# Kernel tuning notes

Measured on AMD Instinct MI355X. Metric: run time of the kernel, lower is better.

The kernel has to match this reference:

```python
import jax, jax.numpy as jnp
import numpy as np

DIM = 256          # channels C
RC = DIM // 8      # reduction_dim = max(dim//8, 4) = 32
K_RATE = 0.75


def setup_inputs() -> dict:
    key = jax.random.key(0)
    ks = jax.random.split(key, 8)
    B, C, H, W = 2, DIM, 64, 64
    rc = RC
    return {
        "x": jax.random.normal(ks[0], (B, C, H, W), jnp.float32),
        "mix_param": jnp.zeros((1,), jnp.float32),                                  # nn.Parameter(zeros(1))
        "w_red": jax.random.normal(ks[1], (rc, C), jnp.float32) * (2.0 / C) ** 0.5,  # conv1x1 kaiming
        "b_red": jnp.zeros((rc,), jnp.float32),
        "w_qkv": jax.random.normal(ks[2], (3 * rc, rc), jnp.float32) * rc ** -0.5,
        "b_qkv": jnp.zeros((3 * rc,), jnp.float32),
        "w_s1": jax.random.normal(ks[3], (C // 2, C), jnp.float32) * C ** -0.5,
        "b_s1": jnp.zeros((C // 2,), jnp.float32),
        "w_s2": jax.random.normal(ks[4], (1, C // 2), jnp.float32) * (C // 2) ** -0.5,
        "b_s2": jnp.zeros((1,), jnp.float32),
    }


def _pool2(x):
    # MaxPool2d(2,2) and AvgPool2d(2,2) on NCHW
    dims, strides = (1, 1, 2, 2), (1, 1, 2, 2)
    mx = jax.lax.reduce_window(x, -jnp.inf, jax.lax.max, dims, strides, 'VALID')
    av = jax.lax.reduce_window(x, 0.0, jax.lax.add, dims, strides, 'VALID') * 0.25
    return mx, av


def _attention(xg, w_red, b_red, w_qkv, b_qkv):
    # xg: [B2, C, h, w]
    B2, C, h, w = xg.shape
    rc = w_red.shape[0]
    S = h * w
    # 1x1 conv channel reduction
    xr = jnp.einsum('bchw,rc->brhw', xg, w_red) + b_red[None, :, None, None]
    xf = xr.reshape(B2, rc, S).transpose(0, 2, 1)             # [B2, S, rc]
    qkv = xf @ w_qkv.T + b_qkv                                # [B2, S, 3*rc]
    q, k, v = qkv[..., :rc], qkv[..., rc:2 * rc], qkv[..., 2 * rc:]
    scores = jnp.einsum('bsr,btr->bst', q, k) / jnp.sqrt(jnp.float32(rc))
    scores = jnp.where(jnp.isnan(scores), -jnp.inf, scores)
    kv = max(1, int(S * K_RATE))                              # static top-k size
    top_vals, top_idx = jax.lax.top_k(scores, kv)             # [B2, S, kv]
    weights = jax.nn.softmax(top_vals, axis=-1)
    # per-(b,s) gather of v rows, then weighted sum over the kv selected keys
    gathered = jax.vmap(lambda vv, ii: vv[ii])(v, top_idx)    # [B2, S, kv, rc]
    out = jnp.einsum('bsk,bskr->bsr', weights, gathered)      # [B2, S, rc]
    out = out.transpose(0, 2, 1).reshape(B2, rc, h, w)
    # re-projection: conv2d with transposed channel_reduction weight, no bias
    return jnp.einsum('brhw,rc->bchw', out, w_red)


def _gating(xg, w_s1, b_s1, w_s2, b_s2):
    # eval-mode gate: hard threshold of sigmoid(score MLP(GAP(x)))
    pooled = xg.mean(axis=(2, 3))                             # [B2, C]
    h1 = jax.nn.relu(pooled @ w_s1.T + b_s1)
    gate_score = jax.nn.sigmoid(h1 @ w_s2.T + b_s2)           # [B2, 1]
    gate = (gate_score > 0.5).astype(xg.dtype)[:, :, None, None]
    return gate * xg


def reference(x, mix_param, w_red, b_red, w_qkv, b_qkv, w_s1, b_s1, w_s2, b_s2):
    mx, av = _pool2(x)
    mw = jax.nn.sigmoid(mix_param)                            # lerp weight, shape [1]
    x1 = mx + mw * (av - mx)                                  # torch.lerp(max, avg, w)
    x2 = av + mw * (mx - av)                                  # torch.lerp(avg, max, w)
    B, C, h, w = x1.shape
    combined = jnp.stack([x1, x2], axis=1).reshape(B * 2, C, h, w)
    attn_out = _attention(combined, w_red, b_red, w_qkv, b_qkv)   # [2B, C, h, w]
    gated = _gating(combined, w_s1, b_s1, w_s2, b_s2).reshape(B, 2, C, h, w)
    out = jnp.maximum(gated[:, 0], gated[:, 1])               # [B, C, h, w]
    return out, attn_out
```

## Files before the change

### kernel.cpp

```cpp
#include <hip/hip_runtime.h>

#define CC 256
#define RC 32
#define SS 1024
#define KV 768

__global__ void k_pool_mix(const float* __restrict__ x, const float* __restrict__ mixp,
                           float* __restrict__ comb, float* __restrict__ pooled) {
    int tid = threadIdx.x;
    int idx = blockIdx.x * 256 + tid;
    int ow = idx & 31, t = idx >> 5;
    int oh = t & 31;  t >>= 5;
    int c = t & 255;  int b = t >> 8;
    const float* px = x + (((size_t)(b*CC + c)*64 + oh*2)*64 + ow*2);
    float2 r0 = *(const float2*)px;
    float2 r1 = *(const float2*)(px + 64);
    float mx = fmaxf(fmaxf(r0.x, r0.y), fmaxf(r1.x, r1.y));
    float av = 0.25f*(r0.x + r0.y + r1.x + r1.y);
    float mw = 1.f/(1.f + expf(-mixp[0]));
    float x1 = mx + mw*(av - mx);
    float x2 = av + mw*(mx - av);
    int s = oh*32 + ow;
    comb[((size_t)(b*2+0)*CC + c)*SS + s] = x1;
    comb[((size_t)(b*2+1)*CC + c)*SS + s] = x2;
    __shared__ float red[256];
    red[tid] = x1; __syncthreads();
    for (int off = 128; off; off >>= 1) { if (tid < off) red[tid] += red[tid+off]; __syncthreads(); }
    if (tid == 0) atomicAdd(&pooled[(b*2)*CC + c], red[0]);
    __syncthreads();
    red[tid] = x2; __syncthreads();
    for (int off = 128; off; off >>= 1) { if (tid < off) red[tid] += red[tid+off]; __syncthreads(); }
    if (tid == 0) atomicAdd(&pooled[(b*2+1)*CC + c], red[0]);
}

__global__ void k_gate(const float* __restrict__ pooled, const float* __restrict__ w_s1,
                       const float* __restrict__ b_s1, const float* __restrict__ w_s2,
                       const float* __restrict__ b_s2, float* __restrict__ gate) {
    int b2 = blockIdx.x; int j = threadIdx.x;
    const float* pl = pooled + b2 * CC;
    float acc = 0.f;
    for (int c = 0; c < CC; c++) acc += pl[c] * w_s1[j*CC + c];
    float h1 = fmaxf(acc * (1.f/1024.f) + b_s1[j], 0.f);
    __shared__ float red[128];
    red[j] = h1 * w_s2[j]; __syncthreads();
    for (int off = 64; off; off >>= 1) { if (j < off) red[j] += red[j+off]; __syncthreads(); }
    if (j == 0) gate[b2] = (red[0] + b_s2[0] > 0.f) ? 1.f : 0.f;
}

__global__ void k_out0(const float* __restrict__ comb, const float* __restrict__ gate,
                       float* __restrict__ out) {
    int idx = blockIdx.x * 256 + threadIdx.x;
    int s = idx & 1023;
    int t = idx >> 10;
    int c = t & 255; int b = t >> 8;
    float g0 = gate[b*2+0], g1 = gate[b*2+1];
    float v0 = g0 * comb[((size_t)(b*2+0)*CC + c)*SS + s];
    float v1 = g1 * comb[((size_t)(b*2+1)*CC + c)*SS + s];
    out[idx] = fmaxf(v0, v1);
}

__global__ __launch_bounds__(256) void k_qkv(
        const float* __restrict__ comb, const float* __restrict__ w_red,
        const float* __restrict__ b_red, const float* __restrict__ w_qkv,
        const float* __restrict__ b_qkv,
        float* __restrict__ q, float* __restrict__ k, float* __restrict__ v) {
    __shared__ float wredT[CC*33];
    __shared__ float wqP[96*33];
    int tid = threadIdx.x;
    int b2 = blockIdx.x >> 6; int tile = blockIdx.x & 63; int s0 = tile*16;
    for (int i = tid; i < CC*RC; i += 256) { int r = i >> 8, c = i & 255; wredT[c*33 + r] = w_red[i]; }
    for (int i = tid; i < 96*RC; i += 256) { int j = i >> 5, r = i & 31; wqP[j*33 + r] = w_qkv[i]; }
    __syncthreads();
    int s_loc = tid >> 4, p = tid & 15;
    int s = s0 + s_loc;
    float xf[RC];
    #pragma unroll
    for (int r = 0; r < RC; r++) xf[r] = 0.f;
    const float* pc = comb + (size_t)(b2*CC)*SS + s;
    #pragma unroll
    for (int ci = 0; ci < 16; ci++) {
        int c = p + 16*ci;
        float val = pc[(size_t)c * SS];
        #pragma unroll
        for (int r = 0; r < RC; r++) xf[r] += val * wredT[c*33 + r];
    }
    #pragma unroll
    for (int m1 = 1; m1 <= 8; m1 <<= 1) {
        #pragma unroll
        for (int r = 0; r < RC; r++) xf[r] += __shfl_xor(xf[r], m1);
    }
    #pragma unroll
    for (int r = 0; r < RC; r++) xf[r] += b_red[r];
    size_t base = (size_t)(b2*SS + s)*RC;
    #pragma unroll
    for (int jj = 0; jj < 6; jj++) {
        int j = p*6 + jj;
        float acc = b_qkv[j];
        #pragma unroll
        for (int r = 0; r < RC; r++) acc += xf[r]*wqP[j*33 + r];
        if      (j < 32) q[base + j]      = acc;
        else if (j < 64) k[base + j - 32] = acc;
        else             v[base + j - 64] = acc;
    }
}

__global__ __launch_bounds__(256, 1) void k_attn(
        const float* __restrict__ qg, const float* __restrict__ kg,
        const float* __restrict__ vg, float* __restrict__ mid) {
    __shared__ float Ks[128*36];
    int tid = threadIdx.x;
    int b2 = blockIdx.x >> 6; int tile = blockIdx.x & 63;
    int r = tid >> 4, c = tid & 15;
    int grow = b2*SS + tile*16 + r;

    float qreg[RC];
    { const float4* qp = (const float4*)(qg + (size_t)grow*RC);
      #pragma unroll
      for (int i = 0; i < 8; i++) { float4 t4 = qp[i]; qreg[4*i]=t4.x; qreg[4*i+1]=t4.y; qreg[4*i+2]=t4.z; qreg[4*i+3]=t4.w; } }

    const float4* ksrc = (const float4*)(kg + (size_t)(b2*SS)*RC);
    const float4* vsrc = (const float4*)(vg + (size_t)(b2*SS)*RC);
    float4 stg[4];
    #pragma unroll
    for (int kk = 0; kk < 4; kk++) stg[kk] = ksrc[tid + 256*kk];

    unsigned int u[64];
    float lmax = -INFINITY;
    const float scale = 0.17677669529663687f;

    #pragma unroll
    for (int ch = 0; ch < 8; ch++) {
        __syncthreads();
        #pragma unroll
        for (int kk = 0; kk < 4; kk++) {
            int idx4 = tid + 256*kk;
            *(float4*)&Ks[(idx4 >> 3)*36 + (idx4 & 7)*4] = stg[kk];
        }
        __syncthreads();
        if (ch < 7) {
            #pragma unroll
            for (int kk = 0; kk < 4; kk++) stg[kk] = ksrc[(ch+1)*1024 + tid + 256*kk];
        } else {
            #pragma unroll
            for (int kk = 0; kk < 4; kk++) stg[kk] = vsrc[tid + 256*kk];
        }
        #pragma unroll
        for (int qq = 0; qq < 8; qq++) {
            int cl = c + 16*qq;
            const float4* kr = (const float4*)&Ks[cl*36];
            float a0=0.f, a1=0.f, a2=0.f, a3=0.f;
            #pragma unroll
            for (int k4 = 0; k4 < 8; k4++) {
                float4 kv4 = kr[k4];
                a0 += qreg[4*k4]*kv4.x;   a1 += qreg[4*k4+1]*kv4.y;
                a2 += qreg[4*k4+2]*kv4.z; a3 += qreg[4*k4+3]*kv4.w;
            }
            float d = ((a0+a1)+(a2+a3))*scale;
            if (d != d) d = -INFINITY;
            lmax = fmaxf(lmax, d);
            unsigned int bb = __float_as_uint(d);
            u[ch*8+qq] = bb ^ ((bb & 0x80000000u) ? 0xFFFFFFFFu : 0x80000000u);
        }
    }

    #pragma unroll
    for (int m1 = 1; m1 <= 8; m1 <<= 1) lmax = fmaxf(lmax, __shfl_xor(lmax, m1));
    float m = lmax;

    unsigned int p = 0u, utau = 0u; bool found = false;
    for (int bit = 31; bit >= 0; --bit) {
        if (found) break;
        unsigned int cand = p | (1u << bit);
        int cnt = 0;
        #pragma unroll
        for (int i = 0; i < 64; i++) cnt += (u[i] >= cand) ? 1 : 0;
        #pragma unroll
        for (int m1 = 1; m1 <= 8; m1 <<= 1) cnt += __shfl_xor(cnt, m1);
        if (cnt >= KV) {
            if (cnt == KV) {
                unsigned int um = 0xFFFFFFFFu;
                #pragma unroll
                for (int i = 0; i < 64; i++) if (u[i] >= cand && u[i] < um) um = u[i];
                #pragma unroll
                for (int m1 = 1; m1 <= 8; m1 <<= 1) {
                    unsigned int o = (unsigned int)__shfl_xor((int)um, m1);
                    um = (o < um) ? o : um;
                }
                utau = um; found = true;
            } else p = cand;
        }
    }
    if (!found) utau = p;

    int cg = 0, eqc = 0;
    #pragma unroll
    for (int i = 0; i < 64; i++) { cg += (u[i] > utau) ? 1 : 0; eqc += (u[i] == utau) ? 1 : 0; }
    #pragma unroll
    for (int m1 = 1; m1 <= 8; m1 <<= 1) { cg += __shfl_xor(cg, m1); eqc += __shfl_xor(eqc, m1); }
    int extra = KV - cg;

    float w[64]; float den = 0.f;
    if (extra == eqc) {
        #pragma unroll
        for (int i = 0; i < 64; i++) {
            bool sel = (u[i] >= utau);
            unsigned int bb = u[i] ^ ((u[i] & 0x80000000u) ? 0x80000000u : 0xFFFFFFFFu);
            float wv = sel ? expf(__uint_as_float(bb) - m) : 0.f;
            w[i] = wv; den += wv;
        }
    } else {
        int prior = 0;
        #pragma unroll
        for (int i = 0; i < 64; i++) {
            bool eq = (u[i] == utau);
            unsigned long long bm = __ballot(eq);
            unsigned int bm16 = (unsigned int)((bm >> (tid & 48)) & 0xFFFFull);
            int rank = prior + __popc(bm16 & ((1u << c) - 1u));
            prior += __popc(bm16);
            bool sel = (u[i] > utau) || (eq && rank < extra);
            unsigned int bb = u[i] ^ ((u[i] & 0x80000000u) ? 0x80000000u : 0xFFFFFFFFu);
            float wv = sel ? expf(__uint_as_float(bb) - m) : 0.f;
            w[i] = wv; den += wv;
        }
    }
    #pragma unroll
    for (int m1 = 1; m1 <= 8; m1 <<= 1) den += __shfl_xor(den, m1);

    float acc[RC];
    #pragma unroll
    for (int i = 0; i < RC; i++) acc[i] = 0.f;
    #pragma unroll
    for (int ch = 0; ch < 8; ch++) {
        __syncthreads();
        #pragma unroll
        for (int kk = 0; kk < 4; kk++) {
            int idx4 = tid + 256*kk;
            *(float4*)&Ks[(idx4 >> 3)*36 + (idx4 & 7)*4] = stg[kk];
        }
        __syncthreads();
        if (ch < 7) {
            #pragma unroll
            for (int kk = 0; kk < 4; kk++) stg[kk] = vsrc[(ch+1)*1024 + tid + 256*kk];
        }
        #pragma unroll
        for (int qq = 0; qq < 8; qq++) {
            int cl = c + 16*qq;
            float wj = w[ch*8 + qq];
            const float4* vr = (const float4*)&Ks[cl*36];
            #pragma unroll
            for (int k4 = 0; k4 < 8; k4++) {
                float4 vv = vr[k4];
                acc[4*k4]   += wj*vv.x; acc[4*k4+1] += wj*vv.y;
                acc[4*k4+2] += wj*vv.z; acc[4*k4+3] += wj*vv.w;
            }
        }
    }
    #pragma unroll
    for (int m1 = 1; m1 <= 8; m1 <<= 1) {
        #pragma unroll
        for (int i = 0; i < RC; i++) acc[i] += __shfl_xor(acc[i], m1);
    }
    if (c == 0) {
        float rden = 1.f/den;
        float4* dst = (float4*)(mid + (size_t)grow*RC);
        #pragma unroll
        for (int k4 = 0; k4 < 8; k4++)
            dst[k4] = make_float4(acc[4*k4]*rden, acc[4*k4+1]*rden, acc[4*k4+2]*rden, acc[4*k4+3]*rden);
    }
}

__global__ __launch_bounds__(256) void k_proj(
        const float* __restrict__ mid, const float* __restrict__ w_red,
        float* __restrict__ attn_out) {
    __shared__ float wr[32*32];
    int tid = threadIdx.x;
    int b2 = blockIdx.x >> 5; int st = (blockIdx.x >> 3) & 3; int cch = blockIdx.x & 7;
    for (int i = tid; i < 1024; i += 256) {
        int rr = i >> 5, cc = i & 31;
        wr[i] = w_red[rr*CC + cch*32 + cc];
    }
    __syncthreads();
    int s = st*256 + tid;
    float xr[RC];
    const float4* mp = (const float4*)(mid + (size_t)(b2*SS + s)*RC);
    #pragma unroll
    for (int i = 0; i < 8; i++) { float4 t4 = mp[i]; xr[4*i]=t4.x; xr[4*i+1]=t4.y; xr[4*i+2]=t4.z; xr[4*i+3]=t4.w; }
    #pragma unroll
    for (int cc = 0; cc < 32; cc++) {
        float a = 0.f;
        #pragma unroll
        for (int rr = 0; rr < RC; rr++) a += xr[rr]*wr[rr*32 + cc];
        attn_out[((size_t)(b2*CC) + cch*32 + cc)*SS + s] = a;
    }
}

extern "C" void kernel_launch(void* const* d_in, const int* in_sizes, int n_in,
                              void* d_out, int out_size, void* d_ws, size_t ws_size,
                              hipStream_t stream) {
    const float* x     = (const float*)d_in[0];
    const float* mixp  = (const float*)d_in[1];
    const float* w_red = (const float*)d_in[2];
    const float* b_red = (const float*)d_in[3];
    const float* w_qkv = (const float*)d_in[4];
    const float* b_qkv = (const float*)d_in[5];
    const float* w_s1  = (const float*)d_in[6];
    const float* b_s1  = (const float*)d_in[7];
    const float* w_s2  = (const float*)d_in[8];
    const float* b_s2  = (const float*)d_in[9];
    float* out = (float*)d_out;

    float* ws     = (float*)d_ws;
    float* comb   = ws;
    float* q      = comb + 1048576;
    float* k      = q + 131072;
    float* v      = k + 131072;
    float* mid    = v + 131072;
    float* pooled = mid + 131072;
    float* gate   = pooled + 1024;

    hipMemsetAsync(pooled, 0, 1024*sizeof(float), stream);
    k_pool_mix<<<2048, 256, 0, stream>>>(x, mixp, comb, pooled);
    k_gate    <<<4,    128, 0, stream>>>(pooled, w_s1, b_s1, w_s2, b_s2, gate);
    k_out0    <<<2048, 256, 0, stream>>>(comb, gate, out);
    k_qkv     <<<256,  256, 0, stream>>>(comb, w_red, b_red, w_qkv, b_qkv, q, k, v);
    k_attn    <<<256,  256, 0, stream>>>(q, k, v, mid);
    k_proj    <<<128,  256, 0, stream>>>(mid, w_red, out + 524288);
}
```

Before: 182.3 us.

## Fuse gating into qkv/proj kernels and use one wavefront per attention row

The pooling kernel now has one block per (batch, channel) and writes the pooled sums directly, which removes the memset and the atomics. The gate MLP runs in four extra blocks of the qkv kernel, and the gated-max output is folded into the projection kernel, cutting the launch count from six to four. The attention kernel now gives each query row one 64-lane wavefront that reads K and V straight from global memory, with no shared-memory staging and no barriers, and runs more blocks per CU. It finishes with a butterfly transpose-reduction of the accumulators instead of the full per-element shuffle reductions. The trade-off is more redundant global/L2 reads of K and V, one per row instead of one per 16-row tile.

```diff
diff --git a/kernel.cpp b/kernel.cpp
--- a/kernel.cpp
+++ b/kernel.cpp
@@ -5,84 +5,94 @@
 #define SS 1024
 #define KV 768
 
-__global__ void k_pool_mix(const float* __restrict__ x, const float* __restrict__ mixp,
-                           float* __restrict__ comb, float* __restrict__ pooled) {
+__global__ __launch_bounds__(256) void k_pool(const float* __restrict__ x,
+                                              const float* __restrict__ mixp,
+                                              float* __restrict__ comb,
+                                              float* __restrict__ pooled) {
+    int bid = blockIdx.x;
+    int b = bid >> 8, c = bid & 255;
     int tid = threadIdx.x;
-    int idx = blockIdx.x * 256 + tid;
-    int ow = idx & 31, t = idx >> 5;
-    int oh = t & 31;  t >>= 5;
-    int c = t & 255;  int b = t >> 8;
-    const float* px = x + (((size_t)(b*CC + c)*64 + oh*2)*64 + ow*2);
-    float2 r0 = *(const float2*)px;
-    float2 r1 = *(const float2*)(px + 64);
-    float mx = fmaxf(fmaxf(r0.x, r0.y), fmaxf(r1.x, r1.y));
-    float av = 0.25f*(r0.x + r0.y + r1.x + r1.y);
-    float mw = 1.f/(1.f + expf(-mixp[0]));
-    float x1 = mx + mw*(av - mx);
-    float x2 = av + mw*(mx - av);
-    int s = oh*32 + ow;
-    comb[((size_t)(b*2+0)*CC + c)*SS + s] = x1;
-    comb[((size_t)(b*2+1)*CC + c)*SS + s] = x2;
-    __shared__ float red[256];
-    red[tid] = x1; __syncthreads();
-    for (int off = 128; off; off >>= 1) { if (tid < off) red[tid] += red[tid+off]; __syncthreads(); }
-    if (tid == 0) atomicAdd(&pooled[(b*2)*CC + c], red[0]);
+    int wid = tid >> 6, lane = tid & 63;
+    const float* base = x + (size_t)(b * CC + c) * 4096;
+    float mw = 1.f / (1.f + expf(-mixp[0]));
+    float* c1 = comb + ((size_t)(b * 2 + 0) * CC + c) * SS;
+    float* c2 = comb + ((size_t)(b * 2 + 1) * CC + c) * SS;
+    float ls1 = 0.f, ls2 = 0.f;
+    #pragma unroll
+    for (int it = 0; it < 4; it++) {
+        int s = tid + 256 * it;
+        int oh = s >> 5, ow = s & 31;
+        const float* px = base + (oh * 2) * 64 + ow * 2;
+        float2 r0 = *(const float2*)px;
+        float2 r1 = *(const float2*)(px + 64);
+        float mx = fmaxf(fmaxf(r0.x, r0.y), fmaxf(r1.x, r1.y));
+        float av = 0.25f * (r0.x + r0.y + r1.x + r1.y);
+        float x1 = mx + mw * (av - mx);
+        float x2 = av + mw * (mx - av);
+        c1[s] = x1; c2[s] = x2;
+        ls1 += x1; ls2 += x2;
+    }
+    #pragma unroll
+    for (int off = 32; off; off >>= 1) {
+        ls1 += __shfl_xor(ls1, off);
+        ls2 += __shfl_xor(ls2, off);
+    }
+    __shared__ float sred[2][4];
+    if (lane == 0) { sred[0][wid] = ls1; sred[1][wid] = ls2; }
     __syncthreads();
-    red[tid] = x2; __syncthreads();
-    for (int off = 128; off; off >>= 1) { if (tid < off) red[tid] += red[tid+off]; __syncthreads(); }
-    if (tid == 0) atomicAdd(&pooled[(b*2+1)*CC + c], red[0]);
-}
-
-__global__ void k_gate(const float* __restrict__ pooled, const float* __restrict__ w_s1,
-                       const float* __restrict__ b_s1, const float* __restrict__ w_s2,
-                       const float* __restrict__ b_s2, float* __restrict__ gate) {
-    int b2 = blockIdx.x; int j = threadIdx.x;
-    const float* pl = pooled + b2 * CC;
-    float acc = 0.f;
-    for (int c = 0; c < CC; c++) acc += pl[c] * w_s1[j*CC + c];
-    float h1 = fmaxf(acc * (1.f/1024.f) + b_s1[j], 0.f);
-    __shared__ float red[128];
-    red[j] = h1 * w_s2[j]; __syncthreads();
-    for (int off = 64; off; off >>= 1) { if (j < off) red[j] += red[j+off]; __syncthreads(); }
-    if (j == 0) gate[b2] = (red[0] + b_s2[0] > 0.f) ? 1.f : 0.f;
-}
-
-__global__ void k_out0(const float* __restrict__ comb, const float* __restrict__ gate,
-                       float* __restrict__ out) {
-    int idx = blockIdx.x * 256 + threadIdx.x;
-    int s = idx & 1023;
-    int t = idx >> 10;
-    int c = t & 255; int b = t >> 8;
-    float g0 = gate[b*2+0], g1 = gate[b*2+1];
-    float v0 = g0 * comb[((size_t)(b*2+0)*CC + c)*SS + s];
-    float v1 = g1 * comb[((size_t)(b*2+1)*CC + c)*SS + s];
-    out[idx] = fmaxf(v0, v1);
+    if (tid == 0) {
+        pooled[(b * 2 + 0) * CC + c] = sred[0][0] + sred[0][1] + sred[0][2] + sred[0][3];
+        pooled[(b * 2 + 1) * CC + c] = sred[1][0] + sred[1][1] + sred[1][2] + sred[1][3];
+    }
 }
 
 __global__ __launch_bounds__(256) void k_qkv(
         const float* __restrict__ comb, const float* __restrict__ w_red,
         const float* __restrict__ b_red, const float* __restrict__ w_qkv,
         const float* __restrict__ b_qkv,
+        const float* __restrict__ pooled, const float* __restrict__ w_s1,
+        const float* __restrict__ b_s1, const float* __restrict__ w_s2,
+        const float* __restrict__ b_s2, float* __restrict__ gate,
         float* __restrict__ q, float* __restrict__ k, float* __restrict__ v) {
-    __shared__ float wredT[CC*33];
-    __shared__ float wqP[96*33];
+    __shared__ float wredT[CC * 33];
+    __shared__ float wqP[96 * 33];
+    __shared__ float gred[128];
     int tid = threadIdx.x;
-    int b2 = blockIdx.x >> 6; int tile = blockIdx.x & 63; int s0 = tile*16;
-    for (int i = tid; i < CC*RC; i += 256) { int r = i >> 8, c = i & 255; wredT[c*33 + r] = w_red[i]; }
-    for (int i = tid; i < 96*RC; i += 256) { int j = i >> 5, r = i & 31; wqP[j*33 + r] = w_qkv[i]; }
+    if (blockIdx.x >= 256) {
+        int b2 = blockIdx.x - 256;
+        if (tid < 128) {
+            const float* pl = pooled + b2 * CC;
+            float acc = 0.f;
+            for (int c = 0; c < CC; c++) acc += pl[c] * w_s1[tid * CC + c];
+            float h1 = fmaxf(acc * (1.f / 1024.f) + b_s1[tid], 0.f);
+            gred[tid] = h1 * w_s2[tid];
+        }
+        __syncthreads();
+        if (tid < 64) gred[tid] += gred[tid + 64];
+        __syncthreads();
+        if (tid == 0) {
+            float sum = 0.f;
+            for (int i = 0; i < 64; i++) sum += gred[i];
+            gate[b2] = (sum + b_s2[0] > 0.f) ? 1.f : 0.f;
+        }
+        return;
+    }
+    int b2 = blockIdx.x >> 6; int tile = blockIdx.x & 63; int s0 = tile * 16;
+    for (int i = tid; i < CC * RC; i += 256) { int r = i >> 8, c = i & 255; wredT[c * 33 + r] = w_red[i]; }
+    for (int i = tid; i < 96 * RC; i += 256) { int j = i >> 5, r = i & 31; wqP[j * 33 + r] = w_qkv[i]; }
     __syncthreads();
     int s_loc = tid >> 4, p = tid & 15;
     int s = s0 + s_loc;
     float xf[RC];
     #pragma unroll
     for (int r = 0; r < RC; r++) xf[r] = 0.f;
-    const float* pc = comb + (size_t)(b2*CC)*SS + s;
+    const float* pc = comb + (size_t)(b2 * CC) * SS + s;
     #pragma unroll
     for (int ci = 0; ci < 16; ci++) {
-        int c = p + 16*ci;
+        int c = p + 16 * ci;
         float val = pc[(size_t)c * SS];
         #pragma unroll
-        for (int r = 0; r < RC; r++) xf[r] += val * wredT[c*33 + r];
+        for (int r = 0; r < RC; r++) xf[r] += val * wredT[c * 33 + r];
     }
     #pragma unroll
     for (int m1 = 1; m1 <= 8; m1 <<= 1) {
@@ -91,80 +101,56 @@
     }
     #pragma unroll
     for (int r = 0; r < RC; r++) xf[r] += b_red[r];
-    size_t base = (size_t)(b2*SS + s)*RC;
+    size_t base = (size_t)(b2 * SS + s) * RC;
     #pragma unroll
     for (int jj = 0; jj < 6; jj++) {
-        int j = p*6 + jj;
+        int j = p * 6 + jj;
         float acc = b_qkv[j];
         #pragma unroll
-        for (int r = 0; r < RC; r++) acc += xf[r]*wqP[j*33 + r];
+        for (int r = 0; r < RC; r++) acc += xf[r] * wqP[j * 33 + r];
         if      (j < 32) q[base + j]      = acc;
         else if (j < 64) k[base + j - 32] = acc;
         else             v[base + j - 64] = acc;
     }
 }
 
-__global__ __launch_bounds__(256, 1) void k_attn(
+__global__ __launch_bounds__(256, 4) void k_attn(
         const float* __restrict__ qg, const float* __restrict__ kg,
         const float* __restrict__ vg, float* __restrict__ mid) {
-    __shared__ float Ks[128*36];
     int tid = threadIdx.x;
-    int b2 = blockIdx.x >> 6; int tile = blockIdx.x & 63;
-    int r = tid >> 4, c = tid & 15;
-    int grow = b2*SS + tile*16 + r;
+    int wid = tid >> 6, lane = tid & 63;
+    int row = blockIdx.x * 4 + wid;
+    int b2 = row >> 10;
+    const float* kbase = kg + ((size_t)b2 << 10) * RC;
+    const float* vbase = vg + ((size_t)b2 << 10) * RC;
 
     float qreg[RC];
-    { const float4* qp = (const float4*)(qg + (size_t)grow*RC);
+    { const float4* qp = (const float4*)(qg + (size_t)row * RC);
       #pragma unroll
-      for (int i = 0; i < 8; i++) { float4 t4 = qp[i]; qreg[4*i]=t4.x; qreg[4*i+1]=t4.y; qreg[4*i+2]=t4.z; qreg[4*i+3]=t4.w; } }
-
-    const float4* ksrc = (const float4*)(kg + (size_t)(b2*SS)*RC);
-    const float4* vsrc = (const float4*)(vg + (size_t)(b2*SS)*RC);
-    float4 stg[4];
-    #pragma unroll
-    for (int kk = 0; kk < 4; kk++) stg[kk] = ksrc[tid + 256*kk];
-
-    unsigned int u[64];
+      for (int i = 0; i < 8; i++) { float4 t = qp[i]; qreg[4*i]=t.x; qreg[4*i+1]=t.y; qreg[4*i+2]=t.z; qreg[4*i+3]=t.w; } }
+
+    const float scale = 0.17677669529663687f;
+    unsigned int u[16];
     float lmax = -INFINITY;
-    const float scale = 0.17677669529663687f;
-
-    #pragma unroll
-    for (int ch = 0; ch < 8; ch++) {
-        __syncthreads();
-        #pragma unroll
-        for (int kk = 0; kk < 4; kk++) {
-            int idx4 = tid + 256*kk;
-            *(float4*)&Ks[(idx4 >> 3)*36 + (idx4 & 7)*4] = stg[kk];
-        }
-        __syncthreads();
-        if (ch < 7) {
-            #pragma unroll
-            for (int kk = 0; kk < 4; kk++) stg[kk] = ksrc[(ch+1)*1024 + tid + 256*kk];
-        } else {
-            #pragma unroll
-            for (int kk = 0; kk < 4; kk++) stg[kk] = vsrc[tid + 256*kk];
-        }
-        #pragma unroll
-        for (int qq = 0; qq < 8; qq++) {
-            int cl = c + 16*qq;
-            const float4* kr = (const float4*)&Ks[cl*36];
-            float a0=0.f, a1=0.f, a2=0.f, a3=0.f;
-            #pragma unroll
-            for (int k4 = 0; k4 < 8; k4++) {
-                float4 kv4 = kr[k4];
-                a0 += qreg[4*k4]*kv4.x;   a1 += qreg[4*k4+1]*kv4.y;
-                a2 += qreg[4*k4+2]*kv4.z; a3 += qreg[4*k4+3]*kv4.w;
-            }
-            float d = ((a0+a1)+(a2+a3))*scale;
-            if (d != d) d = -INFINITY;
-            lmax = fmaxf(lmax, d);
-            unsigned int bb = __float_as_uint(d);
-            u[ch*8+qq] = bb ^ ((bb & 0x80000000u) ? 0xFFFFFFFFu : 0x80000000u);
-        }
-    }
-
-    #pragma unroll
-    for (int m1 = 1; m1 <= 8; m1 <<= 1) lmax = fmaxf(lmax, __shfl_xor(lmax, m1));
+    #pragma unroll
+    for (int i = 0; i < 16; i++) {
+        int col = lane + (i << 6);
+        const float4* kr = (const float4*)(kbase + (size_t)col * RC);
+        float a0 = 0.f, a1 = 0.f, a2 = 0.f, a3 = 0.f;
+        #pragma unroll
+        for (int j = 0; j < 8; j++) {
+            float4 kv = kr[j];
+            a0 += qreg[4*j] * kv.x;   a1 += qreg[4*j+1] * kv.y;
+            a2 += qreg[4*j+2] * kv.z; a3 += qreg[4*j+3] * kv.w;
+        }
+        float d = ((a0 + a1) + (a2 + a3)) * scale;
+        if (d != d) d = -INFINITY;
+        lmax = fmaxf(lmax, d);
+        unsigned int bb = __float_as_uint(d);
+        u[i] = bb ^ ((bb & 0x80000000u) ? 0xFFFFFFFFu : 0x80000000u);
+    }
+    #pragma unroll
+    for (int off = 32; off; off >>= 1) lmax = fmaxf(lmax, __shfl_xor(lmax, off));
     float m = lmax;
 
     unsigned int p = 0u, utau = 0u; bool found = false;
@@ -173,17 +159,17 @@
         unsigned int cand = p | (1u << bit);
         int cnt = 0;
         #pragma unroll
-        for (int i = 0; i < 64; i++) cnt += (u[i] >= cand) ? 1 : 0;
-        #pragma unroll
-        for (int m1 = 1; m1 <= 8; m1 <<= 1) cnt += __shfl_xor(cnt, m1);
+        for (int i = 0; i < 16; i++) cnt += (u[i] >= cand) ? 1 : 0;
+        #pragma unroll
+        for (int off = 1; off <= 32; off <<= 1) cnt += __shfl_xor(cnt, off);
         if (cnt >= KV) {
             if (cnt == KV) {
                 unsigned int um = 0xFFFFFFFFu;
                 #pragma unroll
-                for (int i = 0; i < 64; i++) if (u[i] >= cand && u[i] < um) um = u[i];
+                for (int i = 0; i < 16; i++) if (u[i] >= cand && u[i] < um) um = u[i];
                 #pragma unroll
-                for (int m1 = 1; m1 <= 8; m1 <<= 1) {
-                    unsigned int o = (unsigned int)__shfl_xor((int)um, m1);
+                for (int off = 1; off <= 32; off <<= 1) {
+                    unsigned int o = (unsigned int)__shfl_xor((int)um, off);
                     um = (o < um) ? o : um;
                 }
                 utau = um; found = true;
@@ -194,15 +180,15 @@
 
     int cg = 0, eqc = 0;
     #pragma unroll
-    for (int i = 0; i < 64; i++) { cg += (u[i] > utau) ? 1 : 0; eqc += (u[i] == utau) ? 1 : 0; }
-    #pragma unroll
-    for (int m1 = 1; m1 <= 8; m1 <<= 1) { cg += __shfl_xor(cg, m1); eqc += __shfl_xor(eqc, m1); }
+    for (int i = 0; i < 16; i++) { cg += (u[i] > utau) ? 1 : 0; eqc += (u[i] == utau) ? 1 : 0; }
+    #pragma unroll
+    for (int off = 1; off <= 32; off <<= 1) { cg += __shfl_xor(cg, off); eqc += __shfl_xor(eqc, off); }
     int extra = KV - cg;
 
-    float w[64]; float den = 0.f;
+    float w[16]; float den = 0.f;
     if (extra == eqc) {
         #pragma unroll
-        for (int i = 0; i < 64; i++) {
+        for (int i = 0; i < 16; i++) {
             bool sel = (u[i] >= utau);
             unsigned int bb = u[i] ^ ((u[i] & 0x80000000u) ? 0x80000000u : 0xFFFFFFFFu);
             float wv = sel ? expf(__uint_as_float(bb) - m) : 0.f;
@@ -211,12 +197,11 @@
     } else {
         int prior = 0;
         #pragma unroll
-        for (int i = 0; i < 64; i++) {
+        for (int i = 0; i < 16; i++) {
             bool eq = (u[i] == utau);
             unsigned long long bm = __ballot(eq);
-            unsigned int bm16 = (unsigned int)((bm >> (tid & 48)) & 0xFFFFull);
-            int rank = prior + __popc(bm16 & ((1u << c) - 1u));
-            prior += __popc(bm16);
+            int rank = prior + (int)__popcll(bm & ((1ull << lane) - 1ull));
+            prior += (int)__popcll(bm);
             bool sel = (u[i] > utau) || (eq && rank < extra);
             unsigned int bb = u[i] ^ ((u[i] & 0x80000000u) ? 0x80000000u : 0xFFFFFFFFu);
             float wv = sel ? expf(__uint_as_float(bb) - m) : 0.f;
@@ -224,73 +209,101 @@
         }
     }
     #pragma unroll
-    for (int m1 = 1; m1 <= 8; m1 <<= 1) den += __shfl_xor(den, m1);
+    for (int off = 1; off <= 32; off <<= 1) den += __shfl_xor(den, off);
 
     float acc[RC];
     #pragma unroll
     for (int i = 0; i < RC; i++) acc[i] = 0.f;
     #pragma unroll
-    for (int ch = 0; ch < 8; ch++) {
-        __syncthreads();
-        #pragma unroll
-        for (int kk = 0; kk < 4; kk++) {
-            int idx4 = tid + 256*kk;
-            *(float4*)&Ks[(idx4 >> 3)*36 + (idx4 & 7)*4] = stg[kk];
-        }
-        __syncthreads();
-        if (ch < 7) {
-            #pragma unroll
-            for (int kk = 0; kk < 4; kk++) stg[kk] = vsrc[(ch+1)*1024 + tid + 256*kk];
-        }
-        #pragma unroll
-        for (int qq = 0; qq < 8; qq++) {
-            int cl = c + 16*qq;
-            float wj = w[ch*8 + qq];
-            const float4* vr = (const float4*)&Ks[cl*36];
-            #pragma unroll
-            for (int k4 = 0; k4 < 8; k4++) {
-                float4 vv = vr[k4];
-                acc[4*k4]   += wj*vv.x; acc[4*k4+1] += wj*vv.y;
-                acc[4*k4+2] += wj*vv.z; acc[4*k4+3] += wj*vv.w;
-            }
-        }
-    }
-    #pragma unroll
-    for (int m1 = 1; m1 <= 8; m1 <<= 1) {
-        #pragma unroll
-        for (int i = 0; i < RC; i++) acc[i] += __shfl_xor(acc[i], m1);
-    }
-    if (c == 0) {
-        float rden = 1.f/den;
-        float4* dst = (float4*)(mid + (size_t)grow*RC);
-        #pragma unroll
-        for (int k4 = 0; k4 < 8; k4++)
-            dst[k4] = make_float4(acc[4*k4]*rden, acc[4*k4+1]*rden, acc[4*k4+2]*rden, acc[4*k4+3]*rden);
-    }
+    for (int i = 0; i < 16; i++) {
+        int col = lane + (i << 6);
+        float wj = w[i];
+        const float4* vr = (const float4*)(vbase + (size_t)col * RC);
+        #pragma unroll
+        for (int j = 0; j < 8; j++) {
+            float4 vv = vr[j];
+            acc[4*j]   += wj * vv.x; acc[4*j+1] += wj * vv.y;
+            acc[4*j+2] += wj * vv.z; acc[4*j+3] += wj * vv.w;
+        }
+    }
+    float a16[16];
+    #pragma unroll
+    for (int j = 0; j < 16; j++) {
+        bool hi = (lane & 32) != 0;
+        float keep = hi ? acc[j + 16] : acc[j];
+        float send = hi ? acc[j] : acc[j + 16];
+        a16[j] = keep + __shfl_xor(send, 32);
+    }
+    float a8[8];
+    #pragma unroll
+    for (int j = 0; j < 8; j++) {
+        bool hi = (lane & 16) != 0;
+        float keep = hi ? a16[j + 8] : a16[j];
+        float send = hi ? a16[j] : a16[j + 8];
+        a8[j] = keep + __shfl_xor(send, 16);
+    }
+    float a4[4];
+    #pragma unroll
+    for (int j = 0; j < 4; j++) {
+        bool hi = (lane & 8) != 0;
+        float keep = hi ? a8[j + 4] : a8[j];
+        float send = hi ? a8[j] : a8[j + 4];
+        a4[j] = keep + __shfl_xor(send, 8);
+    }
+    float a2[2];
+    #pragma unroll
+    for (int j = 0; j < 2; j++) {
+        bool hi = (lane & 4) != 0;
+        float keep = hi ? a4[j + 2] : a4[j];
+        float send = hi ? a4[j] : a4[j + 2];
+        a2[j] = keep + __shfl_xor(send, 4);
+    }
+    float a1;
+    {
+        bool hi = (lane & 2) != 0;
+        float keep = hi ? a2[1] : a2[0];
+        float send = hi ? a2[0] : a2[1];
+        a1 = keep + __shfl_xor(send, 2);
+    }
+    float tot = a1 + __shfl_xor(a1, 1);
+    if ((lane & 1) == 0) mid[(size_t)row * RC + (lane >> 1)] = tot / den;
 }
 
 __global__ __launch_bounds__(256) void k_proj(
         const float* __restrict__ mid, const float* __restrict__ w_red,
-        float* __restrict__ attn_out) {
-    __shared__ float wr[32*32];
+        const float* __restrict__ comb, const float* __restrict__ gate,
+        float* __restrict__ out0, float* __restrict__ attn_out) {
     int tid = threadIdx.x;
+    #pragma unroll
+    for (int j = 0; j < 4; j++) {
+        int idx4 = blockIdx.x * 256 + tid + 32768 * j;
+        int b = idx4 >> 16; int c = (idx4 >> 8) & 255; int s4 = idx4 & 255;
+        const float4 v0 = *(const float4*)(comb + (((size_t)(b * 2 + 0) * CC + c) << 10) + s4 * 4);
+        const float4 v1 = *(const float4*)(comb + (((size_t)(b * 2 + 1) * CC + c) << 10) + s4 * 4);
+        float g0 = gate[b * 2 + 0], g1 = gate[b * 2 + 1];
+        float4 o;
+        o.x = fmaxf(g0 * v0.x, g1 * v1.x); o.y = fmaxf(g0 * v0.y, g1 * v1.y);
+        o.z = fmaxf(g0 * v0.z, g1 * v1.z); o.w = fmaxf(g0 * v0.w, g1 * v1.w);
+        *(float4*)(out0 + (size_t)idx4 * 4) = o;
+    }
+    __shared__ float wr[32 * 32];
     int b2 = blockIdx.x >> 5; int st = (blockIdx.x >> 3) & 3; int cch = blockIdx.x & 7;
     for (int i = tid; i < 1024; i += 256) {
         int rr = i >> 5, cc = i & 31;
-        wr[i] = w_red[rr*CC + cch*32 + cc];
+        wr[i] = w_red[rr * CC + cch * 32 + cc];
     }
     __syncthreads();
-    int s = st*256 + tid;
+    int s = st * 256 + tid;
     float xr[RC];
-    const float4* mp = (const float4*)(mid + (size_t)(b2*SS + s)*RC);
+    const float4* mp = (const float4*)(mid + (size_t)(b2 * SS + s) * RC);
     #pragma unroll
     for (int i = 0; i < 8; i++) { float4 t4 = mp[i]; xr[4*i]=t4.x; xr[4*i+1]=t4.y; xr[4*i+2]=t4.z; xr[4*i+3]=t4.w; }
     #pragma unroll
     for (int cc = 0; cc < 32; cc++) {
         float a = 0.f;
         #pragma unroll
-        for (int rr = 0; rr < RC; rr++) a += xr[rr]*wr[rr*32 + cc];
-        attn_out[((size_t)(b2*CC) + cch*32 + cc)*SS + s] = a;
+        for (int rr = 0; rr < RC; rr++) a += xr[rr] * wr[rr * 32 + cc];
+        attn_out[((size_t)(b2 * CC) + cch * 32 + cc) * SS + s] = a;
     }
 }
 
@@ -318,11 +331,9 @@
     float* pooled = mid + 131072;
     float* gate   = pooled + 1024;
 
-    hipMemsetAsync(pooled, 0, 1024*sizeof(float), stream);
-    k_pool_mix<<<2048, 256, 0, stream>>>(x, mixp, comb, pooled);
-    k_gate    <<<4,    128, 0, stream>>>(pooled, w_s1, b_s1, w_s2, b_s2, gate);
-    k_out0    <<<2048, 256, 0, stream>>>(comb, gate, out);
-    k_qkv     <<<256,  256, 0, stream>>>(comb, w_red, b_red, w_qkv, b_qkv, q, k, v);
-    k_attn    <<<256,  256, 0, stream>>>(q, k, v, mid);
-    k_proj    <<<128,  256, 0, stream>>>(mid, w_red, out + 524288);
-}
+    k_pool<<<512,  256, 0, stream>>>(x, mixp, comb, pooled);
+    k_qkv <<<260,  256, 0, stream>>>(comb, w_red, b_red, w_qkv, b_qkv,
+                                     pooled, w_s1, b_s1, w_s2, b_s2, gate, q, k, v);
+    k_attn<<<1024, 256, 0, stream>>>(q, k, v, mid);
+    k_proj<<<128,  256, 0, stream>>>(mid, w_red, comb, gate, out, out + 524288);
+}
```

Result: slower. 243.7 us (+33.7%).
